# Performance work log

Measured on AMD Instinct MI355X. Metric: run time of the kernel, lower is better.

## Reference

```python
import jax, jax.numpy as jnp
import numpy as np

EMBED_DIM = 256
NUM_HEADS = 8
HEAD_DIM = EMBED_DIM // NUM_HEADS
MAX_WAVELENGTH = 10000.0
ROPE_PERCENT = 0.5


def _p_rope(x, positions, head_dim, max_wavelength, rope_percent):
    # x: [BH, N, head_dim]; partial RoPE: rotate only first rope_percent of angle pairs
    half = head_dim // 2
    rope_angles = int(rope_percent * half)
    fraction = 2.0 * jnp.arange(rope_angles, dtype=jnp.float32) / head_dim
    timescale = max_wavelength ** fraction  # [rope_angles]
    sinusoid = positions[:, None] / timescale[None, :]  # [N, rope_angles]
    sin = jnp.sin(sinusoid).astype(x.dtype)
    cos = jnp.cos(sinusoid).astype(x.dtype)
    first, second = jnp.split(x, 2, axis=-1)  # each [BH, N, half]
    f_r, f_p = first[..., :rope_angles], first[..., rope_angles:]
    s_r, s_p = second[..., :rope_angles], second[..., rope_angles:]
    f_out = jnp.concatenate([f_r * cos - s_r * sin, f_p], axis=-1)
    s_out = jnp.concatenate([s_r * cos + f_r * sin, s_p], axis=-1)
    return jnp.concatenate([f_out, s_out], axis=-1)


def setup_inputs() -> dict:
    key = jax.random.key(0)
    ks = jax.random.split(key, 10)
    B, N, D = 2, 4096, EMBED_DIM
    s = 1.0 / np.sqrt(D)
    inp = {
        "hidden_states": jax.random.normal(ks[0], (B, N, D), jnp.float32),
        "q_w": jax.random.normal(ks[1], (D, D), jnp.float32) * s,
        "q_b": jnp.zeros((D,), jnp.float32),
        "k_w": jax.random.normal(ks[2], (D, D), jnp.float32) * s,
        "k_b": jnp.zeros((D,), jnp.float32),
        "v_w": jax.random.normal(ks[3], (D, D), jnp.float32) * s,
        "v_b": jnp.zeros((D,), jnp.float32),
        "o_w": jax.random.normal(ks[4], (D, D), jnp.float32) * s,
        "o_b": jnp.zeros((D,), jnp.float32),
        "attention_biases": jax.random.normal(ks[5], (NUM_HEADS, 2), jnp.float32) * 0.02,
        "num_channels": 8,
        "sequence_length": 512,
    }
    return inp


def reference(hidden_states, q_w, q_b, k_w, k_b, v_w, v_b, o_w, o_b,
              attention_biases, num_channels, sequence_length):
    B, N, D = hidden_states.shape
    H, hd = NUM_HEADS, HEAD_DIM
    scaling = hd ** -0.5

    def shape(t):  # [B,N,D] -> [B*H, N, hd]
        return t.reshape(B, N, H, hd).transpose(0, 2, 1, 3).reshape(B * H, N, hd)

    q = shape(hidden_states @ q_w.T + q_b) * scaling
    k = shape(hidden_states @ k_w.T + k_b)
    v = shape(hidden_states @ v_w.T + v_b)

    positions = jnp.arange(N, dtype=jnp.float32)
    k = _p_rope(k, positions, hd, MAX_WAVELENGTH, ROPE_PERCENT)
    q = _p_rope(q, positions, hd, MAX_WAVELENGTH, ROPE_PERCENT)

    attn = jnp.einsum('bqd,bkd->bqk', q, k).reshape(B, H, N, N)

    variate_ids = jnp.arange(N) // sequence_length
    same = (variate_ids[:, None] == variate_ids[None, :])  # [N,N] bool
    bias_same = attention_biases[:, 0][None, :, None, None]
    bias_diff = attention_biases[:, 1][None, :, None, None]
    attn = attn + jnp.where(same[None, None], bias_same, bias_diff)

    attn = jax.nn.softmax(attn, axis=-1).reshape(B * H, N, N)
    out = jnp.einsum('bqk,bkd->bqd', attn, v)  # [B*H, N, hd]
    out = out.reshape(B, H, N, hd).transpose(0, 2, 1, 3).reshape(B, N, D)
    return out @ o_w.T + o_b
```

## Files before the change

### kernel.cpp

```cpp
#include <hip/hip_runtime.h>
#include <cstdint>
#include <cstddef>

typedef __attribute__((ext_vector_type(8))) short bf16x8;
typedef __attribute__((ext_vector_type(4))) short short4v;
typedef __attribute__((ext_vector_type(4))) float f32x4;
typedef __attribute__((ext_vector_type(2))) unsigned int u32x2;
typedef __attribute__((ext_vector_type(4))) unsigned int u32x4;

extern "C" __device__ float __ocml_native_exp2_f32(float);
#define EXP2 __ocml_native_exp2_f32

__device__ __forceinline__ unsigned cvt_pk_bf16(float a, float b) {
  unsigned r;
  asm("v_cvt_pk_bf16_f32 %0, %1, %2" : "=v"(r) : "v"(a), "v"(b));
  return r;
}

__device__ __forceinline__ short f2bf(float f) {
  unsigned u = __float_as_uint(f);
  u += 0x7FFFu + ((u >> 16) & 1u);
  return (short)(u >> 16);
}

__constant__ float INV_TS[8] = {
  1.0f, 0.5623413251903491f, 0.31622776601683794f, 0.17782794100389228f,
  0.1f, 0.05623413251903491f, 0.031622776601683794f, 0.017782794100389228f
};

__global__ __launch_bounds__(256) void gemm_qkv_rope(
    const float* __restrict__ X,
    const float* __restrict__ W0, const float* __restrict__ W1, const float* __restrict__ W2,
    const float* __restrict__ b0, const float* __restrict__ b1, const float* __restrict__ b2,
    short* __restrict__ Qo, short* __restrict__ Ko, short* __restrict__ Vt)
{
  __shared__ short sA[128 * 40];
  __shared__ short sB[64 * 40];
  const int t = threadIdx.x;
  const int w = t >> 6, l = t & 63;
  const int l15 = l & 15, lg = l >> 4;
  const int rbase = blockIdx.x * 128;
  const int cgbase = blockIdx.y * 64;
  const int mat = cgbase >> 8;
  const float* W = (mat == 0) ? W0 : ((mat == 1) ? W1 : W2);
  const float* bias = (mat == 0) ? b0 : ((mat == 1) ? b1 : b2);
  const int wbase = cgbase & 255;

  const int ar = t >> 1, akc = (t & 1) * 16;
  const int br = t >> 2, bkc = (t & 3) * 8;

  const float* Bg = W + (size_t)(wbase + br) * 256 + bkc;
  const float* Agf = X + (size_t)(rbase + ar) * 256 + akc;

  const int wr = w >> 1, wc = w & 1;

  f32x4 acc[4][2];
#pragma unroll
  for (int i = 0; i < 4; ++i) {
    acc[i][0] = {0.f, 0.f, 0.f, 0.f};
    acc[i][1] = {0.f, 0.f, 0.f, 0.f};
  }

  for (int k0 = 0; k0 < 256; k0 += 32) {
    f32x4 a0 = *(const f32x4*)(Agf + k0);
    f32x4 a1 = *(const f32x4*)(Agf + k0 + 4);
    f32x4 a2 = *(const f32x4*)(Agf + k0 + 8);
    f32x4 a3 = *(const f32x4*)(Agf + k0 + 12);
    u32x4 pa0, pa1;
    pa0.x = cvt_pk_bf16(a0[0], a0[1]); pa0.y = cvt_pk_bf16(a0[2], a0[3]);
    pa0.z = cvt_pk_bf16(a1[0], a1[1]); pa0.w = cvt_pk_bf16(a1[2], a1[3]);
    pa1.x = cvt_pk_bf16(a2[0], a2[1]); pa1.y = cvt_pk_bf16(a2[2], a2[3]);
    pa1.z = cvt_pk_bf16(a3[0], a3[1]); pa1.w = cvt_pk_bf16(a3[2], a3[3]);
    f32x4 bv0 = *(const f32x4*)(Bg + k0);
    f32x4 bv1 = *(const f32x4*)(Bg + k0 + 4);
    u32x4 pb;
    pb.x = cvt_pk_bf16(bv0[0], bv0[1]); pb.y = cvt_pk_bf16(bv0[2], bv0[3]);
    pb.z = cvt_pk_bf16(bv1[0], bv1[1]); pb.w = cvt_pk_bf16(bv1[2], bv1[3]);

    __syncthreads();
    *(u32x4*)(sA + ar * 40 + akc)     = pa0;
    *(u32x4*)(sA + ar * 40 + akc + 8) = pa1;
    *(u32x4*)(sB + br * 40 + bkc)     = pb;
    __syncthreads();

    bf16x8 af[4], bfr[2];
#pragma unroll
    for (int i = 0; i < 4; ++i)
      af[i] = *(const bf16x8*)(sA + (wr * 64 + i * 16 + l15) * 40 + lg * 8);
#pragma unroll
    for (int j = 0; j < 2; ++j)
      bfr[j] = *(const bf16x8*)(sB + (wc * 32 + j * 16 + l15) * 40 + lg * 8);
#pragma unroll
    for (int i = 0; i < 4; ++i)
#pragma unroll
      for (int j = 0; j < 2; ++j)
        acc[i][j] = __builtin_amdgcn_mfma_f32_16x16x32_bf16(af[i], bfr[j], acc[i][j], 0, 0, 0);
  }

  const int cm = wbase + wc * 32;
  const int hh = cm >> 5;
  const float bv0 = bias[cm + l15];
  const float bv1 = bias[cm + 16 + l15];
  const float SCL_Q = 0.17677669529663687f;

#pragma unroll
  for (int i = 0; i < 4; ++i) {
    const int m0 = rbase + wr * 64 + i * 16 + lg * 4;
    const int b = m0 >> 12, n0 = m0 & 4095;
    if (mat < 2) {
      short* dst = (mat == 0 ? Qo : Ko) + (size_t)(b * 8 + hh) * 131072 + (size_t)n0 * 32 + l15;
#pragma unroll
      for (int jj = 0; jj < 4; ++jj) {
        float v0 = acc[i][0][jj] + bv0;
        float v1 = acc[i][1][jj] + bv1;
        if (mat == 0) { v0 *= SCL_Q; v1 *= SCL_Q; }
        if (l15 < 8) {
          float ang = (float)(n0 + jj) * INV_TS[l15];
          float s = sinf(ang), c = cosf(ang);
          float r0 = v0 * c - v1 * s;
          float r1 = v1 * c + v0 * s;
          v0 = r0; v1 = r1;
        }
        dst[jj * 32]      = f2bf(v0);
        dst[jj * 32 + 16] = f2bf(v1);
      }
    } else {
      short* dstv = Vt + (size_t)(b * 8 + hh) * 131072 + n0;
#pragma unroll
      for (int j = 0; j < 2; ++j) {
        const float bv = j ? bv1 : bv0;
        short4v pk;
#pragma unroll
        for (int jj = 0; jj < 4; ++jj) pk[jj] = f2bf(acc[i][j][jj] + bv);
        *(short4v*)(dstv + (size_t)(j * 16 + l15) * 4096) = pk;
      }
    }
  }
}

__global__ __launch_bounds__(256, 4) void attn_fwd(
    const short* __restrict__ Qg, const short* __restrict__ Kg, const short* __restrict__ Vg,
    const float* __restrict__ ab, const int* __restrict__ slp,
    float* __restrict__ Op, float* __restrict__ denp)
{
  __shared__ short sK[2][64 * 40];
  __shared__ short sV[2][32 * 72];
  __shared__ short sP[4][32 * 72];
  const int t = threadIdx.x, w = t >> 6, l = t & 63;
  const int l15 = l & 15, lg = l >> 4;
  const int bh = blockIdx.y, h = bh & 7;
  const int z = blockIdx.z;
  const int qb = blockIdx.x * 128 + w * 32;
  const int sl = *slp;

  const short* Qb = Qg + (size_t)bh * (4096 * 32);
  const short* Kb = Kg + (size_t)bh * (4096 * 32);
  const short* Vb = Vg + (size_t)bh * (32 * 4096);

  bf16x8 qf[2];
  qf[0] = *(const bf16x8*)(Qb + (size_t)(qb + l15) * 32 + lg * 8);
  qf[1] = *(const bf16x8*)(Qb + (size_t)(qb + 16 + l15) * 32 + lg * 8);

  const float LOG2E = 1.4426950408889634f;
  const float lbs = ab[h * 2] * LOG2E, lbd = ab[h * 2 + 1] * LOG2E;
  const int qv[2]  = { (qb + l15) / sl, (qb + 16 + l15) / sl };
  const int qlo[2] = { qv[0] * sl, qv[1] * sl };

  short* P = &sP[w][0];
  short* pw = P + l15 * 72 + lg * 4;
  const short* pr = P + l15 * 72 + lg * 8;

  const f32x4 fz = {0.f, 0.f, 0.f, 0.f};
  f32x4 Oacc[2][2];
  Oacc[0][0] = fz; Oacc[0][1] = fz; Oacc[1][0] = fz; Oacc[1][1] = fz;
  float den[2] = {0.f, 0.f};

  const int kt0 = z * 32, kt1 = kt0 + 32;
  const int kstart = kt0 * 64;

  const int kr = t >> 2, kc0 = (t & 3) * 8;
  const int vd = t >> 3, vk0 = (t & 7) * 8;
  const short* kg = Kb + (size_t)(kstart + kr) * 32 + kc0;
  const short* vg = Vb + (size_t)vd * 4096 + kstart + vk0;

  bf16x8 krg = *(const bf16x8*)kg;
  bf16x8 vrg = *(const bf16x8*)vg;
  *(bf16x8*)(&sK[0][0] + kr * 40 + kc0) = krg;
  *(bf16x8*)(&sV[0][0] + vd * 72 + vk0) = vrg;
  kg += 64 * 32; vg += 64;
  krg = *(const bf16x8*)kg;
  vrg = *(const bf16x8*)vg;
  __syncthreads();

  int kv = kstart / sl;
  int rem = (kv + 1) * sl - kstart;
  int cur = 0;

#pragma unroll 2
  for (int kt = kt0; kt < kt1; ++kt) {
    *(bf16x8*)(&sK[cur ^ 1][0] + kr * 40 + kc0) = krg;
    *(bf16x8*)(&sV[cur ^ 1][0] + vd * 72 + vk0) = vrg;
    const int adv = (kt + 2 < kt1) ? 1 : 0;
    kg += adv * (64 * 32); vg += adv * 64;
    krg = *(const bf16x8*)kg;
    vrg = *(const bf16x8*)vg;

    const short* sKc = &sK[cur][0];
    const short* sVc = &sV[cur][0];

    f32x4 S[2][4];
#pragma unroll
    for (int t4 = 0; t4 < 4; ++t4) {
      bf16x8 kf = *(const bf16x8*)(sKc + (t4 * 16 + l15) * 40 + lg * 8);
      S[0][t4] = __builtin_amdgcn_mfma_f32_16x16x32_bf16(kf, qf[0], fz, 0, 0, 0);
      S[1][t4] = __builtin_amdgcn_mfma_f32_16x16x32_bf16(kf, qf[1], fz, 0, 0, 0);
    }

    const int kb0 = kt * 64;
    if (rem >= 64) {
      float lb[2];
      lb[0] = (qv[0] == kv) ? lbs : lbd;
      lb[1] = (qv[1] == kv) ? lbs : lbd;
#pragma unroll
      for (int g = 0; g < 2; ++g)
#pragma unroll
        for (int t4 = 0; t4 < 4; ++t4) {
          float p0 = EXP2(S[g][t4][0] * LOG2E + lb[g]);
          float p1 = EXP2(S[g][t4][1] * LOG2E + lb[g]);
          float p2 = EXP2(S[g][t4][2] * LOG2E + lb[g]);
          float p3 = EXP2(S[g][t4][3] * LOG2E + lb[g]);
          den[g] += (p0 + p1) + (p2 + p3);
          u32x2 u; u.x = cvt_pk_bf16(p0, p1); u.y = cvt_pk_bf16(p2, p3);
          *(u32x2*)(pw + g * 1152 + t4 * 16) = u;
        }
    } else {
#pragma unroll
      for (int g = 0; g < 2; ++g)
#pragma unroll
        for (int t4 = 0; t4 < 4; ++t4) {
          const int gk = kb0 + t4 * 16 + lg * 4;
          float p[4];
#pragma unroll
          for (int j = 0; j < 4; ++j) {
            float lb = ((unsigned)(gk + j - qlo[g]) < (unsigned)sl) ? lbs : lbd;
            p[j] = EXP2(S[g][t4][j] * LOG2E + lb);
            den[g] += p[j];
          }
          u32x2 u; u.x = cvt_pk_bf16(p[0], p[1]); u.y = cvt_pk_bf16(p[2], p[3]);
          *(u32x2*)(pw + g * 1152 + t4 * 16) = u;
        }
    }
    rem -= 64;
    while (rem <= 0) { kv += 1; rem += sl; }

#pragma unroll
    for (int g = 0; g < 2; ++g)
#pragma unroll
      for (int kk = 0; kk < 2; ++kk) {
        bf16x8 pf = *(const bf16x8*)(pr + g * 1152 + kk * 32);
        bf16x8 vf0 = *(const bf16x8*)(sVc + l15 * 72 + kk * 32 + lg * 8);
        bf16x8 vf1 = *(const bf16x8*)(sVc + (16 + l15) * 72 + kk * 32 + lg * 8);
        Oacc[g][0] = __builtin_amdgcn_mfma_f32_16x16x32_bf16(pf, vf0, Oacc[g][0], 0, 0, 0);
        Oacc[g][1] = __builtin_amdgcn_mfma_f32_16x16x32_bf16(pf, vf1, Oacc[g][1], 0, 0, 0);
      }

    __syncthreads();
    cur ^= 1;
  }

#pragma unroll
  for (int g = 0; g < 2; ++g) {
    den[g] += __shfl_xor(den[g], 16, 64);
    den[g] += __shfl_xor(den[g], 32, 64);
  }

  const size_t zb = ((size_t)z * 16 + bh) * 4096;
  if (lg == 0) {
#pragma unroll
    for (int g = 0; g < 2; ++g)
      denp[zb + qb + g * 16 + l15] = den[g];
  }
#pragma unroll
  for (int g = 0; g < 2; ++g)
#pragma unroll
    for (int nt = 0; nt < 2; ++nt)
#pragma unroll
      for (int j = 0; j < 4; ++j) {
        const int n = qb + g * 16 + lg * 4 + j;
        Op[(zb + n) * 32 + nt * 16 + l15] = Oacc[g][nt][j];
      }
}

__global__ __launch_bounds__(256) void combine(
    const float* __restrict__ Op, const float* __restrict__ denp,
    short* __restrict__ attno)
{
  const int id = blockIdx.x * 256 + threadIdx.x;
  const int d4 = (id & 7) * 4;
  const int n  = (id >> 3) & 4095;
  const int bh = id >> 15;
  const size_t base = ((size_t)bh * 4096 + n) * 32 + d4;
  const size_t zoff = (size_t)16 * 4096 * 32;
  f32x4 o0 = *(const f32x4*)(Op + base);
  f32x4 o1 = *(const f32x4*)(Op + zoff + base);
  const float rd = 1.0f / (denp[bh * 4096 + n] + denp[16 * 4096 + bh * 4096 + n]);
  const int b = bh >> 3, hh = bh & 7;
  u32x2 u;
  u.x = cvt_pk_bf16((o0[0] + o1[0]) * rd, (o0[1] + o1[1]) * rd);
  u.y = cvt_pk_bf16((o0[2] + o1[2]) * rd, (o0[3] + o1[3]) * rd);
  *(u32x2*)(attno + ((size_t)(b * 4096 + n) * 256 + hh * 32 + d4)) = u;
}

template<int A_BF16, int OUT_BF16>
__global__ __launch_bounds__(256) void gemm_mfma(
    const void* __restrict__ Ain,
    const float* __restrict__ W0, const float* __restrict__ W1, const float* __restrict__ W2,
    const float* __restrict__ b0, const float* __restrict__ b1, const float* __restrict__ b2,
    void* __restrict__ Cout, int Ntot)
{
  __shared__ short sA[128 * 40];
  __shared__ short sB[64 * 40];
  const int t = threadIdx.x;
  const int w = t >> 6, l = t & 63;
  const int l15 = l & 15, lg = l >> 4;
  const int rbase = blockIdx.x * 128;
  const int cgbase = blockIdx.y * 64;
  const int mat = cgbase >> 8;
  const float* W = (mat == 0) ? W0 : ((mat == 1) ? W1 : W2);
  const float* bias = (mat == 0) ? b0 : ((mat == 1) ? b1 : b2);
  const int wbase = cgbase & 255;

  const int ar = t >> 1, akc = (t & 1) * 16;
  const int br = t >> 2, bkc = (t & 3) * 8;

  const float* Bg = W + (size_t)(wbase + br) * 256 + bkc;
  const float* Agf = (const float*)Ain + (size_t)(rbase + ar) * 256 + akc;
  const short* Agh = (const short*)Ain + (size_t)(rbase + ar) * 256 + akc;

  const int wr = w >> 1, wc = w & 1;

  f32x4 acc[4][2];
#pragma unroll
  for (int i = 0; i < 4; ++i) {
    acc[i][0] = {0.f, 0.f, 0.f, 0.f};
    acc[i][1] = {0.f, 0.f, 0.f, 0.f};
  }

  for (int k0 = 0; k0 < 256; k0 += 32) {
    u32x4 pa0, pa1;
    if constexpr (A_BF16) {
      pa0 = *(const u32x4*)(Agh + k0);
      pa1 = *(const u32x4*)(Agh + k0 + 8);
    } else {
      f32x4 a0 = *(const f32x4*)(Agf + k0);
      f32x4 a1 = *(const f32x4*)(Agf + k0 + 4);
      f32x4 a2 = *(const f32x4*)(Agf + k0 + 8);
      f32x4 a3 = *(const f32x4*)(Agf + k0 + 12);
      pa0.x = cvt_pk_bf16(a0[0], a0[1]); pa0.y = cvt_pk_bf16(a0[2], a0[3]);
      pa0.z = cvt_pk_bf16(a1[0], a1[1]); pa0.w = cvt_pk_bf16(a1[2], a1[3]);
      pa1.x = cvt_pk_bf16(a2[0], a2[1]); pa1.y = cvt_pk_bf16(a2[2], a2[3]);
      pa1.z = cvt_pk_bf16(a3[0], a3[1]); pa1.w = cvt_pk_bf16(a3[2], a3[3]);
    }
    f32x4 bv0 = *(const f32x4*)(Bg + k0);
    f32x4 bv1 = *(const f32x4*)(Bg + k0 + 4);
    u32x4 pb;
    pb.x = cvt_pk_bf16(bv0[0], bv0[1]); pb.y = cvt_pk_bf16(bv0[2], bv0[3]);
    pb.z = cvt_pk_bf16(bv1[0], bv1[1]); pb.w = cvt_pk_bf16(bv1[2], bv1[3]);

    __syncthreads();
    *(u32x4*)(sA + ar * 40 + akc)     = pa0;
    *(u32x4*)(sA + ar * 40 + akc + 8) = pa1;
    *(u32x4*)(sB + br * 40 + bkc)     = pb;
    __syncthreads();

    bf16x8 af[4], bfr[2];
#pragma unroll
    for (int i = 0; i < 4; ++i)
      af[i] = *(const bf16x8*)(sA + (wr * 64 + i * 16 + l15) * 40 + lg * 8);
#pragma unroll
    for (int j = 0; j < 2; ++j)
      bfr[j] = *(const bf16x8*)(sB + (wc * 32 + j * 16 + l15) * 40 + lg * 8);
#pragma unroll
    for (int i = 0; i < 4; ++i)
#pragma unroll
      for (int j = 0; j < 2; ++j)
        acc[i][j] = __builtin_amdgcn_mfma_f32_16x16x32_bf16(af[i], bfr[j], acc[i][j], 0, 0, 0);
  }

#pragma unroll
  for (int i = 0; i < 4; ++i)
#pragma unroll
    for (int j = 0; j < 2; ++j) {
      const int n = cgbase + wc * 32 + j * 16 + l15;
      const float bv = bias[wbase + wc * 32 + j * 16 + l15];
#pragma unroll
      for (int jj = 0; jj < 4; ++jj) {
        const size_t m = (size_t)(rbase + wr * 64 + i * 16 + lg * 4 + jj);
        const float val = acc[i][j][jj] + bv;
        if constexpr (OUT_BF16) ((short*)Cout)[m * Ntot + n] = f2bf(val);
        else                    ((float*)Cout)[m * Ntot + n] = val;
      }
    }
}

extern "C" void kernel_launch(void* const* d_in, const int* in_sizes, int n_in,
                              void* d_out, int out_size, void* d_ws, size_t ws_size,
                              hipStream_t stream) {
  (void)in_sizes; (void)n_in; (void)out_size; (void)ws_size;
  const float* hs = (const float*)d_in[0];
  const float* qw = (const float*)d_in[1];
  const float* qb = (const float*)d_in[2];
  const float* kw = (const float*)d_in[3];
  const float* kb = (const float*)d_in[4];
  const float* vw = (const float*)d_in[5];
  const float* vb = (const float*)d_in[6];
  const float* ow = (const float*)d_in[7];
  const float* ob = (const float*)d_in[8];
  const float* ab = (const float*)d_in[9];
  const int* sl   = (const int*)d_in[11];
  float* out = (float*)d_out;

  char* ws = (char*)d_ws;
  float* Op   = (float*)(ws);
  short* Qbf  = (short*)(ws + 16777216);
  short* Kbf  = (short*)(ws + 20971520);
  short* Vtb  = (short*)(ws + 25165824);
  float* denp = (float*)(ws + 29360128);
  short* attno= (short*)(ws + 29884416);

  gemm_qkv_rope<<<dim3(64, 12), 256, 0, stream>>>(hs, qw, kw, vw, qb, kb, vb, Qbf, Kbf, Vtb);
  attn_fwd<<<dim3(32, 16, 2), 256, 0, stream>>>(Qbf, Kbf, Vtb, ab, sl, Op, denp);
  combine<<<dim3(2048), 256, 0, stream>>>(Op, denp, attno);
  gemm_mfma<1, 0><<<dim3(64, 4), 256, 0, stream>>>(attno, ow, ow, ow, ob, ob, ob, out, 256);
}
```

Baseline: 94.56 us.

## Keep softmax P in registers and feed PV via 16x16x16 bf16 MFMA

```diff
diff --git a/kernel.cpp b/kernel.cpp
--- a/kernel.cpp
+++ b/kernel.cpp
@@ -21,6 +21,18 @@
   unsigned u = __float_as_uint(f);
   u += 0x7FFFu + ((u >> 16) & 1u);
   return (short)(u >> 16);
+}
+
+__device__ __forceinline__ f32x4 mfma16(short4v a, short4v b, f32x4 c) {
+#if __has_builtin(__builtin_amdgcn_mfma_f32_16x16x16bf16_1k)
+  return __builtin_amdgcn_mfma_f32_16x16x16bf16_1k(a, b, c, 0, 0, 0);
+#elif __has_builtin(__builtin_amdgcn_mfma_f32_16x16x16_bf16)
+  return __builtin_amdgcn_mfma_f32_16x16x16_bf16(a, b, c, 0, 0, 0);
+#else
+  bf16x8 a8 = {a[0], a[1], a[2], a[3], 0, 0, 0, 0};
+  bf16x8 b8 = {b[0], b[1], b[2], b[3], 0, 0, 0, 0};
+  return __builtin_amdgcn_mfma_f32_16x16x32_bf16(a8, b8, c, 0, 0, 0);
+#endif
 }
 
 __constant__ float INV_TS[8] = {
@@ -138,14 +150,13 @@
   }
 }
 
-__global__ __launch_bounds__(256, 4) void attn_fwd(
+__global__ __launch_bounds__(256) void attn_fwd(
     const short* __restrict__ Qg, const short* __restrict__ Kg, const short* __restrict__ Vg,
     const float* __restrict__ ab, const int* __restrict__ slp,
     float* __restrict__ Op, float* __restrict__ denp)
 {
   __shared__ short sK[2][64 * 40];
   __shared__ short sV[2][32 * 72];
-  __shared__ short sP[4][32 * 72];
   const int t = threadIdx.x, w = t >> 6, l = t & 63;
   const int l15 = l & 15, lg = l >> 4;
   const int bh = blockIdx.y, h = bh & 7;
@@ -165,10 +176,6 @@
   const float lbs = ab[h * 2] * LOG2E, lbd = ab[h * 2 + 1] * LOG2E;
   const int qv[2]  = { (qb + l15) / sl, (qb + 16 + l15) / sl };
   const int qlo[2] = { qv[0] * sl, qv[1] * sl };
-
-  short* P = &sP[w][0];
-  short* pw = P + l15 * 72 + lg * 4;
-  const short* pr = P + l15 * 72 + lg * 8;
 
   const f32x4 fz = {0.f, 0.f, 0.f, 0.f};
   f32x4 Oacc[2][2];
@@ -208,6 +215,13 @@
     const short* sKc = &sK[cur][0];
     const short* sVc = &sV[cur][0];
 
+    short4v vB[4][2];
+#pragma unroll
+    for (int t4 = 0; t4 < 4; ++t4)
+#pragma unroll
+      for (int nt = 0; nt < 2; ++nt)
+        vB[t4][nt] = *(const short4v*)(sVc + (nt * 16 + l15) * 72 + t4 * 16 + lg * 4);
+
     f32x4 S[2][4];
 #pragma unroll
     for (int t4 = 0; t4 < 4; ++t4) {
@@ -216,6 +230,7 @@
       S[1][t4] = __builtin_amdgcn_mfma_f32_16x16x32_bf16(kf, qf[1], fz, 0, 0, 0);
     }
 
+    short4v pA[2][4];
     const int kb0 = kt * 64;
     if (rem >= 64) {
       float lb[2];
@@ -231,7 +246,7 @@
           float p3 = EXP2(S[g][t4][3] * LOG2E + lb[g]);
           den[g] += (p0 + p1) + (p2 + p3);
           u32x2 u; u.x = cvt_pk_bf16(p0, p1); u.y = cvt_pk_bf16(p2, p3);
-          *(u32x2*)(pw + g * 1152 + t4 * 16) = u;
+          pA[g][t4] = __builtin_bit_cast(short4v, u);
         }
     } else {
 #pragma unroll
@@ -247,21 +262,18 @@
             den[g] += p[j];
           }
           u32x2 u; u.x = cvt_pk_bf16(p[0], p[1]); u.y = cvt_pk_bf16(p[2], p[3]);
-          *(u32x2*)(pw + g * 1152 + t4 * 16) = u;
+          pA[g][t4] = __builtin_bit_cast(short4v, u);
         }
     }
     rem -= 64;
     while (rem <= 0) { kv += 1; rem += sl; }
 
 #pragma unroll
-    for (int g = 0; g < 2; ++g)
-#pragma unroll
-      for (int kk = 0; kk < 2; ++kk) {
-        bf16x8 pf = *(const bf16x8*)(pr + g * 1152 + kk * 32);
-        bf16x8 vf0 = *(const bf16x8*)(sVc + l15 * 72 + kk * 32 + lg * 8);
-        bf16x8 vf1 = *(const bf16x8*)(sVc + (16 + l15) * 72 + kk * 32 + lg * 8);
-        Oacc[g][0] = __builtin_amdgcn_mfma_f32_16x16x32_bf16(pf, vf0, Oacc[g][0], 0, 0, 0);
-        Oacc[g][1] = __builtin_amdgcn_mfma_f32_16x16x32_bf16(pf, vf1, Oacc[g][1], 0, 0, 0);
+    for (int t4 = 0; t4 < 4; ++t4)
+#pragma unroll
+      for (int g = 0; g < 2; ++g) {
+        Oacc[g][0] = mfma16(pA[g][t4], vB[t4][0], Oacc[g][0]);
+        Oacc[g][1] = mfma16(pA[g][t4], vB[t4][1], Oacc[g][1]);
       }
 
     __syncthreads();
```

New measurement: 100.1 us. 1.06x slower.
